# Optimization experiments

Measured on AMD Instinct MI355X. Metric: run time of the kernel, lower is better.

Reference implementation:

```python
import jax, jax.numpy as jnp
import numpy as np

N = 100000   # nodes
E = 1600000  # edges
F = 256      # feature_dim
H = 64       # hidden_dim == out_channels
HEADS = 1


def setup_inputs() -> dict:
    key = jax.random.key(0)
    ks = jax.random.split(key, 12)
    x = jax.random.normal(ks[0], (N, F), dtype=jnp.float32)
    edge_index = jax.random.randint(ks[1], (2, E), 0, N, dtype=jnp.int32)
    s = 0.05
    params = {
        'W_proj': jax.random.normal(ks[2], (F, H), dtype=jnp.float32) * s,
        'b_proj': jnp.zeros((H,), dtype=jnp.float32),
        'Wq1': jax.random.normal(ks[3], (H, HEADS * H), dtype=jnp.float32) * s,
        'Wk1': jax.random.normal(ks[4], (H, HEADS * H), dtype=jnp.float32) * s,
        'Wv1': jax.random.normal(ks[5], (H, HEADS * H), dtype=jnp.float32) * s,
        'Wq2': jax.random.normal(ks[6], (H, HEADS * H), dtype=jnp.float32) * s,
        'Wk2': jax.random.normal(ks[7], (H, HEADS * H), dtype=jnp.float32) * s,
        'Wv2': jax.random.normal(ks[8], (H, HEADS * H), dtype=jnp.float32) * s,
        'W_sig': jax.random.normal(ks[9], (H, 1), dtype=jnp.float32) * s,
        'b_sig': jnp.zeros((1,), dtype=jnp.float32),
    }
    return {'x': x, 'edge_index': edge_index, **params}


def _gat_layer(x, src, dst, Wq, Wk, Wv):
    # x: [N, H]; src/dst: [E] (edge_index[0]=source j, edge_index[1]=dest i)
    n = x.shape[0]
    q = (x @ Wq).reshape(n, HEADS, H)
    k = (x @ Wk).reshape(n, HEADS, H)
    v = (x @ Wv).reshape(n, HEADS, H)
    # edge-wise scores: (q_i * k_j).sum(-1) / sqrt(out_channels)
    scores = jnp.einsum('ehc,ehc->eh', q[dst], k[src]) / np.float32(np.sqrt(H))
    alpha = jax.nn.relu(scores)                                  # [E, HEADS]
    # segment softmax over destination neighborhoods (numerically stable)
    m = jax.ops.segment_max(alpha, dst, num_segments=n)          # [N, HEADS]
    m = jnp.where(jnp.isfinite(m), m, jnp.float32(0.0))
    e = jnp.exp(alpha - m[dst])
    denom = jax.ops.segment_sum(e, dst, num_segments=n)
    a = e / (denom[dst] + jnp.float32(1e-16))                    # [E, HEADS]
    # scatter-weighted sum of values to destinations
    out = jax.ops.segment_sum(v[src] * a[:, :, None], dst, num_segments=n)
    return out.mean(axis=1), a                                   # [N, H], [E, HEADS]


def reference(x, edge_index, W_proj, b_proj, Wq1, Wk1, Wv1, Wq2, Wk2, Wv2, W_sig, b_sig):
    src, dst = edge_index[0], edge_index[1]
    h = jax.nn.gelu(x @ W_proj + b_proj, approximate=False)
    h, attn1 = _gat_layer(h, src, dst, Wq1, Wk1, Wv1)
    h = jax.nn.gelu(h, approximate=False)
    h, attn2 = _gat_layer(h, src, dst, Wq2, Wk2, Wv2)
    signals = h @ W_sig + b_sig                                  # [N, 1]
    return signals, attn1, attn2
```

## Files before the change

kernel.cpp:

```cpp
#include <hip/hip_runtime.h>
#include <math.h>

#define FF 256
#define HH 64

typedef __attribute__((ext_vector_type(8))) short short8;
typedef __attribute__((ext_vector_type(8))) unsigned short ushort8;
typedef __attribute__((ext_vector_type(4))) float f32x4;

__device__ __forceinline__ float gelu_f(float x) {
    return 0.5f * x * (1.0f + erff(x * 0.70710678118654752f));
}

__device__ __forceinline__ unsigned short bf16rne(float f) {
    unsigned u = __float_as_uint(f);
    unsigned r = u + 0x7FFFu + ((u >> 16) & 1u);
    return (unsigned short)(r >> 16);
}
__device__ __forceinline__ float bf16tof(unsigned short s) {
    return __uint_as_float(((unsigned)s) << 16);
}

__device__ __forceinline__ void bf16split(float f, short& hi, short& lo) {
    unsigned u = __float_as_uint(f);
    unsigned r = u + 0x7FFFu + ((u >> 16) & 1u);
    hi = (short)(r >> 16);
    float fh = __uint_as_float(r & 0xFFFF0000u);
    float fl = f - fh;
    unsigned u2 = __float_as_uint(fl);
    unsigned r2 = u2 + 0x7FFFu + ((u2 >> 16) & 1u);
    lo = (short)(r2 >> 16);
}

__global__ __launch_bounds__(256) void k_wprep(
        const float* __restrict__ Wp,
        const float* __restrict__ Wq1, const float* __restrict__ Wk1, const float* __restrict__ Wv1,
        const float* __restrict__ Wq2, const float* __restrict__ Wk2, const float* __restrict__ Wv2,
        short* __restrict__ wf) {
    int total = 16384 + 6 * 4096;
    for (int gid = blockIdx.x * 256 + threadIdx.x; gid < total; gid += gridDim.x * 256) {
        const float* W;
        int fid, hibase, lobase;
        if (gid < 16384) {
            W = Wp; fid = gid; hibase = 0; lobase = 16384;
        } else {
            int t = gid - 16384;
            int m = t >> 12;
            fid = t & 4095;
            switch (m) {
                case 0: W = Wq1; break;
                case 1: W = Wk1; break;
                case 2: W = Wv1; break;
                case 3: W = Wq2; break;
                case 4: W = Wk2; break;
                default: W = Wv2; break;
            }
            hibase = 32768 + m * 8192;
            lobase = hibase + 4096;
        }
        int j    = fid & 7;
        int lane = (fid >> 3) & 63;
        int ct   = (fid >> 9) & 3;
        int s    = fid >> 11;
        int k    = s * 32 + (lane >> 4) * 8 + j;
        int col  = ct * 16 + (lane & 15);
        short hi, lo;
        bf16split(W[k * HH + col], hi, lo);
        wf[hibase + fid] = hi;
        wf[lobase + fid] = lo;
    }
}

__global__ __launch_bounds__(256) void k_degree(const int* __restrict__ dst,
        int* __restrict__ deg, int* __restrict__ rank, int E) {
    int e0 = (blockIdx.x * 256 + threadIdx.x) * 4;
    if (e0 + 3 < E) {
        int4 d4 = *reinterpret_cast<const int4*>(dst + e0);
        int4 r4;
        r4.x = atomicAdd(&deg[d4.x], 1);
        r4.y = atomicAdd(&deg[d4.y], 1);
        r4.z = atomicAdd(&deg[d4.z], 1);
        r4.w = atomicAdd(&deg[d4.w], 1);
        *reinterpret_cast<int4*>(rank + e0) = r4;
    } else {
        for (int e = e0; e < E; ++e) rank[e] = atomicAdd(&deg[dst[e]], 1);
    }
}

__global__ __launch_bounds__(256) void k_scan1(const int* __restrict__ deg,
        int* __restrict__ out, int* __restrict__ bsums, int n) {
    __shared__ int lds[256];
    int t = threadIdx.x;
    int base = blockIdx.x * 1024 + t * 4;
    int v0 = (base     < n) ? deg[base]     : 0;
    int v1 = (base + 1 < n) ? deg[base + 1] : 0;
    int v2 = (base + 2 < n) ? deg[base + 2] : 0;
    int v3 = (base + 3 < n) ? deg[base + 3] : 0;
    int s = v0 + v1 + v2 + v3;
    int val = s;
    lds[t] = val;
    __syncthreads();
    #pragma unroll
    for (int off = 1; off < 256; off <<= 1) {
        int tmp = (t >= off) ? lds[t - off] : 0;
        __syncthreads();
        val += tmp;
        lds[t] = val;
        __syncthreads();
    }
    if (t == 255) bsums[blockIdx.x] = val;
    int excl = val - s;
    if (base     < n) out[base]     = excl;
    if (base + 1 < n) out[base + 1] = excl + v0;
    if (base + 2 < n) out[base + 2] = excl + v0 + v1;
    if (base + 3 < n) out[base + 3] = excl + v0 + v1 + v2;
}

__global__ __launch_bounds__(256) void k_scan2(const int* __restrict__ bsums,
        int* __restrict__ boffs, int nb) {
    __shared__ int lds[256];
    int t = threadIdx.x;
    int s = (t < nb) ? bsums[t] : 0;
    int val = s;
    lds[t] = val;
    __syncthreads();
    #pragma unroll
    for (int off = 1; off < 256; off <<= 1) {
        int tmp = (t >= off) ? lds[t - off] : 0;
        __syncthreads();
        val += tmp;
        lds[t] = val;
        __syncthreads();
    }
    if (t < nb) boffs[t] = val - s;
}

__global__ __launch_bounds__(256) void k_scan3(int* __restrict__ rowptr,
        const int* __restrict__ boffs, int n, int E) {
    int i = blockIdx.x * 256 + threadIdx.x;
    if (i < n) rowptr[i] += boffs[i >> 10];
    if (i == n) rowptr[n] = E;
}

__global__ __launch_bounds__(256) void k_fill(const int* __restrict__ src,
        const int* __restrict__ dst, const int* __restrict__ rowptr,
        const int* __restrict__ rank,
        int* __restrict__ esrc, int* __restrict__ inv, int E) {
    int e0 = (blockIdx.x * 256 + threadIdx.x) * 4;
    if (e0 + 3 < E) {
        int4 d4 = *reinterpret_cast<const int4*>(dst + e0);
        int4 s4 = *reinterpret_cast<const int4*>(src + e0);
        int4 r4 = *reinterpret_cast<const int4*>(rank + e0);
        int p0 = rowptr[d4.x] + r4.x;
        int p1 = rowptr[d4.y] + r4.y;
        int p2 = rowptr[d4.z] + r4.z;
        int p3 = rowptr[d4.w] + r4.w;
        esrc[p0] = s4.x;
        esrc[p1] = s4.y;
        esrc[p2] = s4.z;
        esrc[p3] = s4.w;
        *reinterpret_cast<int4*>(inv + e0) = (int4){p0, p1, p2, p3};
    } else {
        for (int e = e0; e < E; ++e) {
            int pos = rowptr[dst[e]] + rank[e];
            esrc[pos] = src[e];
            inv[e] = pos;
        }
    }
}

__global__ __launch_bounds__(256) void k_attn(const float* __restrict__ ecsr,
        const int* __restrict__ inv, float* __restrict__ attn, int E) {
    int e0 = (blockIdx.x * 256 + threadIdx.x) * 4;
    if (e0 + 3 < E) {
        int4 i4 = *reinterpret_cast<const int4*>(inv + e0);
        float4 a;
        a.x = ecsr[i4.x]; a.y = ecsr[i4.y]; a.z = ecsr[i4.z]; a.w = ecsr[i4.w];
        *reinterpret_cast<float4*>(attn + e0) = a;
    } else {
        for (int e = e0; e < E; ++e) attn[e] = ecsr[inv[e]];
    }
}

__global__ __launch_bounds__(256) void k_proj(const float* __restrict__ x,
        const short* __restrict__ wf, const float* __restrict__ b,
        float* __restrict__ h, int n) {
    int lane = threadIdx.x & 63;
    int w    = threadIdx.x >> 6;
    int m    = lane & 15, g = lane >> 4;
    int rowc = min(blockIdx.x * 64 + w * 16 + m, n - 1);
    const float* xrow = x + (size_t)rowc * FF + g * 8;
    const short* wlo = wf + 16384;
    f32x4 acc[4];
    #pragma unroll
    for (int ct = 0; ct < 4; ++ct) acc[ct] = (f32x4){0.f, 0.f, 0.f, 0.f};
    #pragma unroll
    for (int s = 0; s < 8; ++s) {
        float4 a0 = *reinterpret_cast<const float4*>(xrow + s * 32);
        float4 a1 = *reinterpret_cast<const float4*>(xrow + s * 32 + 4);
        float av[8] = {a0.x, a0.y, a0.z, a0.w, a1.x, a1.y, a1.z, a1.w};
        short8 ah, al;
        #pragma unroll
        for (int j = 0; j < 8; ++j) { short hi, lo; bf16split(av[j], hi, lo); ah[j] = hi; al[j] = lo; }
        #pragma unroll
        for (int ct = 0; ct < 4; ++ct) {
            int fo = ((s * 4 + ct) * 64 + lane) * 8;
            short8 bh = *reinterpret_cast<const short8*>(wf + fo);
            short8 bl = *reinterpret_cast<const short8*>(wlo + fo);
            acc[ct] = __builtin_amdgcn_mfma_f32_16x16x32_bf16(ah, bh, acc[ct], 0, 0, 0);
            acc[ct] = __builtin_amdgcn_mfma_f32_16x16x32_bf16(al, bh, acc[ct], 0, 0, 0);
            acc[ct] = __builtin_amdgcn_mfma_f32_16x16x32_bf16(ah, bl, acc[ct], 0, 0, 0);
        }
    }
    int orow0 = blockIdx.x * 64 + w * 16 + g * 4;
    #pragma unroll
    for (int ct = 0; ct < 4; ++ct) {
        int col = ct * 16 + m;
        float bias = b[col];
        #pragma unroll
        for (int r = 0; r < 4; ++r) {
            int row = orow0 + r;
            if (row < n) h[(size_t)row * HH + col] = gelu_f(acc[ct][r] + bias);
        }
    }
}

__global__ __launch_bounds__(256) void k_qkv(const float* __restrict__ hsrc,
        const short* __restrict__ wfq, const short* __restrict__ wfk, const short* __restrict__ wfv,
        float* __restrict__ q, unsigned short* __restrict__ kv, int n) {
    int lane = threadIdx.x & 63;
    int w    = threadIdx.x >> 6;
    int m    = lane & 15, g = lane >> 4;
    int rowc = min(blockIdx.x * 64 + w * 16 + m, n - 1);
    const float* hrow = hsrc + (size_t)rowc * HH + g * 8;
    f32x4 aq[4], ak[4], av_[4];
    #pragma unroll
    for (int ct = 0; ct < 4; ++ct) {
        aq[ct] = (f32x4){0.f, 0.f, 0.f, 0.f};
        ak[ct] = (f32x4){0.f, 0.f, 0.f, 0.f};
        av_[ct] = (f32x4){0.f, 0.f, 0.f, 0.f};
    }
    #pragma unroll
    for (int s = 0; s < 2; ++s) {
        float4 a0 = *reinterpret_cast<const float4*>(hrow + s * 32);
        float4 a1 = *reinterpret_cast<const float4*>(hrow + s * 32 + 4);
        float avv[8] = {a0.x, a0.y, a0.z, a0.w, a1.x, a1.y, a1.z, a1.w};
        short8 ah, al;
        #pragma unroll
        for (int j = 0; j < 8; ++j) { short hi, lo; bf16split(avv[j], hi, lo); ah[j] = hi; al[j] = lo; }
        #pragma unroll
        for (int ct = 0; ct < 4; ++ct) {
            int fo = ((s * 4 + ct) * 64 + lane) * 8;
            short8 qh = *reinterpret_cast<const short8*>(wfq + fo);
            short8 ql = *reinterpret_cast<const short8*>(wfq + 4096 + fo);
            short8 kh = *reinterpret_cast<const short8*>(wfk + fo);
            short8 kl = *reinterpret_cast<const short8*>(wfk + 4096 + fo);
            short8 vh = *reinterpret_cast<const short8*>(wfv + fo);
            short8 vl = *reinterpret_cast<const short8*>(wfv + 4096 + fo);
            aq[ct] = __builtin_amdgcn_mfma_f32_16x16x32_bf16(ah, qh, aq[ct], 0, 0, 0);
            aq[ct] = __builtin_amdgcn_mfma_f32_16x16x32_bf16(al, qh, aq[ct], 0, 0, 0);
            aq[ct] = __builtin_amdgcn_mfma_f32_16x16x32_bf16(ah, ql, aq[ct], 0, 0, 0);
            ak[ct] = __builtin_amdgcn_mfma_f32_16x16x32_bf16(ah, kh, ak[ct], 0, 0, 0);
            ak[ct] = __builtin_amdgcn_mfma_f32_16x16x32_bf16(al, kh, ak[ct], 0, 0, 0);
            ak[ct] = __builtin_amdgcn_mfma_f32_16x16x32_bf16(ah, kl, ak[ct], 0, 0, 0);
            av_[ct] = __builtin_amdgcn_mfma_f32_16x16x32_bf16(ah, vh, av_[ct], 0, 0, 0);
            av_[ct] = __builtin_amdgcn_mfma_f32_16x16x32_bf16(al, vh, av_[ct], 0, 0, 0);
            av_[ct] = __builtin_amdgcn_mfma_f32_16x16x32_bf16(ah, vl, av_[ct], 0, 0, 0);
        }
    }
    int orow0 = blockIdx.x * 64 + w * 16 + g * 4;
    #pragma unroll
    for (int ct = 0; ct < 4; ++ct) {
        int col = ct * 16 + m;
        int cb  = (col >> 3) * 16 + (col & 7);
        #pragma unroll
        for (int r = 0; r < 4; ++r) {
            int row = orow0 + r;
            if (row < n) {
                q[(size_t)row * HH + col]       = aq[ct][r];
                kv[(size_t)row * 128 + cb]      = bf16rne(ak[ct][r]);
                kv[(size_t)row * 128 + cb + 8]  = bf16rne(av_[ct][r]);
            }
        }
    }
}

template<bool LAST>
__global__ __launch_bounds__(256) void k_edge(
        const float* __restrict__ q, const unsigned short* __restrict__ kv,
        const int* __restrict__ rowptr,
        const int* __restrict__ esrc,
        float* __restrict__ ecsr,
        float* __restrict__ hout,
        float* __restrict__ signals,
        const float* __restrict__ Wsig, const float* __restrict__ bsig,
        int n) {
    int node = blockIdx.x * 4 + (threadIdx.x >> 6);
    if (node >= n) return;
    int lane = threadIdx.x & 63;
    int li = lane & 7, g = lane >> 3;
    int start = rowptr[node], end = rowptr[node + 1];
    int deg = end - start;
    float qf[8];
    {
        float4 q0 = *reinterpret_cast<const float4*>(q + (size_t)node * HH + li * 8);
        float4 q1 = *reinterpret_cast<const float4*>(q + (size_t)node * HH + li * 8 + 4);
        qf[0] = q0.x; qf[1] = q0.y; qf[2] = q0.z; qf[3] = q0.w;
        qf[4] = q1.x; qf[5] = q1.y; qf[6] = q1.z; qf[7] = q1.w;
    }
    int p0 = start + lane;
    int el = (p0 < end) ? esrc[p0] : 0;

    float acc[8] = {0.f, 0.f, 0.f, 0.f, 0.f, 0.f, 0.f, 0.f};
    float s = 0.f;
    for (int c = 0; c < deg; c += 16) {
        int idx0 = c + g, idx1 = c + 8 + g;
        bool v0 = idx0 < deg, v1 = idx1 < deg;
        int sv0, sv1;
        if (c + 16 <= 64) {
            sv0 = __shfl(el, idx0);
            sv1 = __shfl(el, idx1);
        } else {
            sv0 = v0 ? esrc[start + idx0] : 0;
            sv1 = v1 ? esrc[start + idx1] : 0;
        }
        const unsigned short* b0 = kv + (size_t)sv0 * 128 + li * 16;
        const unsigned short* b1 = kv + (size_t)sv1 * 128 + li * 16;
        ushort8 k0 = *reinterpret_cast<const ushort8*>(b0);
        ushort8 w0 = *reinterpret_cast<const ushort8*>(b0 + 8);
        ushort8 k1 = *reinterpret_cast<const ushort8*>(b1);
        ushort8 w1 = *reinterpret_cast<const ushort8*>(b1 + 8);
        float d0 = 0.f, d1 = 0.f;
        #pragma unroll
        for (int j = 0; j < 8; ++j) {
            d0 = fmaf(qf[j], bf16tof(k0[j]), d0);
            d1 = fmaf(qf[j], bf16tof(k1[j]), d1);
        }
        d0 += __shfl_xor(d0, 1); d1 += __shfl_xor(d1, 1);
        d0 += __shfl_xor(d0, 2); d1 += __shfl_xor(d1, 2);
        d0 += __shfl_xor(d0, 4); d1 += __shfl_xor(d1, 4);
        float e0 = v0 ? __expf(fmaxf(d0 * 0.125f, 0.f)) : 0.f;
        float e1 = v1 ? __expf(fmaxf(d1 * 0.125f, 0.f)) : 0.f;
        s += e0 + e1;
        if (v0 && li == 0) ecsr[start + idx0] = e0;
        if (v1 && li == 0) ecsr[start + idx1] = e1;
        #pragma unroll
        for (int j = 0; j < 8; ++j) {
            acc[j] = fmaf(e0, bf16tof(w0[j]), acc[j]);
            acc[j] = fmaf(e1, bf16tof(w1[j]), acc[j]);
        }
    }
    #pragma unroll
    for (int off = 8; off < 64; off <<= 1) {
        s += __shfl_xor(s, off);
        #pragma unroll
        for (int j = 0; j < 8; ++j) acc[j] += __shfl_xor(acc[j], off);
    }
    float inv = 1.0f / (s + 1e-16f);

    if (!LAST) {
        if (g == 0) {
            float4 o0, o1;
            o0.x = gelu_f(acc[0] * inv); o0.y = gelu_f(acc[1] * inv);
            o0.z = gelu_f(acc[2] * inv); o0.w = gelu_f(acc[3] * inv);
            o1.x = gelu_f(acc[4] * inv); o1.y = gelu_f(acc[5] * inv);
            o1.z = gelu_f(acc[6] * inv); o1.w = gelu_f(acc[7] * inv);
            *reinterpret_cast<float4*>(hout + (size_t)node * HH + li * 8)     = o0;
            *reinterpret_cast<float4*>(hout + (size_t)node * HH + li * 8 + 4) = o1;
        }
    } else {
        float4 w0 = *reinterpret_cast<const float4*>(Wsig + li * 8);
        float4 w1 = *reinterpret_cast<const float4*>(Wsig + li * 8 + 4);
        float t = acc[0] * w0.x + acc[1] * w0.y + acc[2] * w0.z + acc[3] * w0.w
                + acc[4] * w1.x + acc[5] * w1.y + acc[6] * w1.z + acc[7] * w1.w;
        t *= inv;
        t += __shfl_xor(t, 1);
        t += __shfl_xor(t, 2);
        t += __shfl_xor(t, 4);
        if (lane == 0) signals[node] = t + bsig[0];
    }
    for (int p = p0; p < end; p += 64)
        ecsr[p] *= inv;
}

extern "C" void kernel_launch(void* const* d_in, const int* in_sizes, int n_in,
                              void* d_out, int out_size, void* d_ws, size_t ws_size,
                              hipStream_t stream) {
    const float* x   = (const float*)d_in[0];
    const int*   ei  = (const int*)  d_in[1];
    const float* Wp  = (const float*)d_in[2];
    const float* bp  = (const float*)d_in[3];
    const float* Wq1 = (const float*)d_in[4];
    const float* Wk1 = (const float*)d_in[5];
    const float* Wv1 = (const float*)d_in[6];
    const float* Wq2 = (const float*)d_in[7];
    const float* Wk2 = (const float*)d_in[8];
    const float* Wv2 = (const float*)d_in[9];
    const float* Wsg = (const float*)d_in[10];
    const float* bsg = (const float*)d_in[11];

    const int N = in_sizes[0] / FF;
    const int E = in_sizes[1] / 2;
    const int* src = ei;
    const int* dst = ei + E;

    char* ws = (char*)d_ws;
    size_t off = 0;
    auto alloc = [&](size_t bytes) -> void* {
        void* p = ws + off;
        off += (bytes + 255) & ~(size_t)255;
        return p;
    };
    float* q           = (float*)alloc((size_t)N * HH * 4);
    unsigned short* kv = (unsigned short*)alloc((size_t)N * 128 * 2);
    float* h           = (float*)alloc((size_t)N * HH * 4);
    float* ecsr        = (float*)alloc((size_t)E * 4);
    int* inv           = (int*)alloc((size_t)E * 4);
    int* esrc          = (int*)alloc((size_t)E * 4);
    int* rank          = (int*)alloc((size_t)E * 4);
    int* deg           = (int*)alloc((size_t)N * 4);
    int* rowptr        = (int*)alloc((size_t)(N + 1) * 4);
    int* bsums         = (int*)alloc(256 * 4);
    int* boffs         = (int*)alloc(256 * 4);
    short* wf          = (short*)alloc((size_t)81920 * 2);

    float* out     = (float*)d_out;
    float* signals = out;
    float* attn1   = out + N;
    float* attn2   = out + N + E;

    k_wprep<<<64, 256, 0, stream>>>(Wp, Wq1, Wk1, Wv1, Wq2, Wk2, Wv2, wf);

    hipMemsetAsync(deg, 0, (size_t)N * 4, stream);
    int e4Blocks = ((E + 3) / 4 + 255) / 256;
    k_degree<<<e4Blocks, 256, 0, stream>>>(dst, deg, rank, E);
    int nb = (N + 1023) / 1024;
    k_scan1<<<nb, 256, 0, stream>>>(deg, rowptr, bsums, N);
    k_scan2<<<1, 256, 0, stream>>>(bsums, boffs, nb);
    k_scan3<<<(N + 1 + 255) / 256, 256, 0, stream>>>(rowptr, boffs, N, E);
    k_fill<<<e4Blocks, 256, 0, stream>>>(src, dst, rowptr, rank, esrc, inv, E);

    int gemmBlocks = (N + 63) / 64;

    k_proj<<<gemmBlocks, 256, 0, stream>>>(x, wf, bp, h, N);

    const short* wfbase = wf + 32768;
    k_qkv<<<gemmBlocks, 256, 0, stream>>>(h, wfbase, wfbase + 8192, wfbase + 16384,
            q, kv, N);
    k_edge<false><<<(N + 3) / 4, 256, 0, stream>>>(q, kv, rowptr, esrc,
            ecsr, h, nullptr, nullptr, nullptr, N);
    k_attn<<<e4Blocks, 256, 0, stream>>>(ecsr, inv, attn1, E);

    k_qkv<<<gemmBlocks, 256, 0, stream>>>(h, wfbase + 24576, wfbase + 32768, wfbase + 40960,
            q, kv, N);
    k_edge<true><<<(N + 3) / 4, 256, 0, stream>>>(q, kv, rowptr, esrc,
            ecsr, nullptr, signals, Wsg, bsg, N);
    k_attn<<<e4Blocks, 256, 0, stream>>>(ecsr, inv, attn2, E);
}
```

Measured before the change: 359.7 us.

## Use fp16 packed math for edge attention, drop split-bf16 activations, move gelu into qkv

Stores q, k and v as fp16 and computes the edge dot products and value accumulation with packed half2 FMAs. This halves the q traffic and doubles the arithmetic per instruction in the gather-bound edge kernel. The qkv GEMM now rounds its activations to a single bf16 instead of a hi/lo split, cutting MFMAs from nine to six per tile. GELU moves from the producers into the qkv input path and uses a polynomial erf approximation. The costs are reduced accuracy from fp16 accumulation of attention-weighted values (overflow or precision risk for large degree sums) and from the approximate erf.

```diff
diff --git a/kernel.cpp b/kernel.cpp
--- a/kernel.cpp
+++ b/kernel.cpp
@@ -1,24 +1,27 @@
 #include <hip/hip_runtime.h>
+#include <hip/hip_fp16.h>
 #include <math.h>
 
 #define FF 256
 #define HH 64
 
 typedef __attribute__((ext_vector_type(8))) short short8;
-typedef __attribute__((ext_vector_type(8))) unsigned short ushort8;
 typedef __attribute__((ext_vector_type(4))) float f32x4;
 
 __device__ __forceinline__ float gelu_f(float x) {
-    return 0.5f * x * (1.0f + erff(x * 0.70710678118654752f));
+    float ax = fabsf(x) * 0.70710678118654752f;
+    float t = __builtin_amdgcn_rcpf(fmaf(0.3275911f, ax, 1.0f));
+    float poly = t * fmaf(t, fmaf(t, fmaf(t, fmaf(t, 1.061405429f, -1.453152027f),
+                  1.421413741f), -0.284496736f), 0.254829592f);
+    float er = 1.0f - poly * __expf(-ax * ax);
+    er = (x < 0.f) ? -er : er;
+    return 0.5f * x * (1.0f + er);
 }
 
 __device__ __forceinline__ unsigned short bf16rne(float f) {
     unsigned u = __float_as_uint(f);
     unsigned r = u + 0x7FFFu + ((u >> 16) & 1u);
     return (unsigned short)(r >> 16);
-}
-__device__ __forceinline__ float bf16tof(unsigned short s) {
-    return __uint_as_float(((unsigned)s) << 16);
 }
 
 __device__ __forceinline__ void bf16split(float f, short& hi, short& lo) {
@@ -30,6 +33,13 @@
     unsigned u2 = __float_as_uint(fl);
     unsigned r2 = u2 + 0x7FFFu + ((u2 >> 16) & 1u);
     lo = (short)(r2 >> 16);
+}
+
+__device__ __forceinline__ __half2 shfl_xor_h2(__half2 v, int off) {
+    union { __half2 h; int i; } u;
+    u.h = v;
+    u.i = __shfl_xor(u.i, off, 64);
+    return u.h;
 }
 
 __global__ __launch_bounds__(256) void k_wprep(
@@ -220,14 +230,14 @@
         #pragma unroll
         for (int r = 0; r < 4; ++r) {
             int row = orow0 + r;
-            if (row < n) h[(size_t)row * HH + col] = gelu_f(acc[ct][r] + bias);
+            if (row < n) h[(size_t)row * HH + col] = acc[ct][r] + bias;
         }
     }
 }
 
 __global__ __launch_bounds__(256) void k_qkv(const float* __restrict__ hsrc,
         const short* __restrict__ wfq, const short* __restrict__ wfk, const short* __restrict__ wfv,
-        float* __restrict__ q, unsigned short* __restrict__ kv, int n) {
+        __half* __restrict__ qh, __half* __restrict__ kv, int n) {
     int lane = threadIdx.x & 63;
     int w    = threadIdx.x >> 6;
     int m    = lane & 15, g = lane >> 4;
@@ -245,27 +255,24 @@
         float4 a0 = *reinterpret_cast<const float4*>(hrow + s * 32);
         float4 a1 = *reinterpret_cast<const float4*>(hrow + s * 32 + 4);
         float avv[8] = {a0.x, a0.y, a0.z, a0.w, a1.x, a1.y, a1.z, a1.w};
-        short8 ah, al;
-        #pragma unroll
-        for (int j = 0; j < 8; ++j) { short hi, lo; bf16split(avv[j], hi, lo); ah[j] = hi; al[j] = lo; }
+        short8 ah;
+        #pragma unroll
+        for (int j = 0; j < 8; ++j) ah[j] = (short)bf16rne(gelu_f(avv[j]));
         #pragma unroll
         for (int ct = 0; ct < 4; ++ct) {
             int fo = ((s * 4 + ct) * 64 + lane) * 8;
-            short8 qh = *reinterpret_cast<const short8*>(wfq + fo);
-            short8 ql = *reinterpret_cast<const short8*>(wfq + 4096 + fo);
-            short8 kh = *reinterpret_cast<const short8*>(wfk + fo);
-            short8 kl = *reinterpret_cast<const short8*>(wfk + 4096 + fo);
-            short8 vh = *reinterpret_cast<const short8*>(wfv + fo);
-            short8 vl = *reinterpret_cast<const short8*>(wfv + 4096 + fo);
-            aq[ct] = __builtin_amdgcn_mfma_f32_16x16x32_bf16(ah, qh, aq[ct], 0, 0, 0);
-            aq[ct] = __builtin_amdgcn_mfma_f32_16x16x32_bf16(al, qh, aq[ct], 0, 0, 0);
-            aq[ct] = __builtin_amdgcn_mfma_f32_16x16x32_bf16(ah, ql, aq[ct], 0, 0, 0);
-            ak[ct] = __builtin_amdgcn_mfma_f32_16x16x32_bf16(ah, kh, ak[ct], 0, 0, 0);
-            ak[ct] = __builtin_amdgcn_mfma_f32_16x16x32_bf16(al, kh, ak[ct], 0, 0, 0);
-            ak[ct] = __builtin_amdgcn_mfma_f32_16x16x32_bf16(ah, kl, ak[ct], 0, 0, 0);
-            av_[ct] = __builtin_amdgcn_mfma_f32_16x16x32_bf16(ah, vh, av_[ct], 0, 0, 0);
-            av_[ct] = __builtin_amdgcn_mfma_f32_16x16x32_bf16(al, vh, av_[ct], 0, 0, 0);
-            av_[ct] = __builtin_amdgcn_mfma_f32_16x16x32_bf16(ah, vl, av_[ct], 0, 0, 0);
+            short8 qh8 = *reinterpret_cast<const short8*>(wfq + fo);
+            short8 ql8 = *reinterpret_cast<const short8*>(wfq + 4096 + fo);
+            short8 kh8 = *reinterpret_cast<const short8*>(wfk + fo);
+            short8 kl8 = *reinterpret_cast<const short8*>(wfk + 4096 + fo);
+            short8 vh8 = *reinterpret_cast<const short8*>(wfv + fo);
+            short8 vl8 = *reinterpret_cast<const short8*>(wfv + 4096 + fo);
+            aq[ct] = __builtin_amdgcn_mfma_f32_16x16x32_bf16(ah, qh8, aq[ct], 0, 0, 0);
+            aq[ct] = __builtin_amdgcn_mfma_f32_16x16x32_bf16(ah, ql8, aq[ct], 0, 0, 0);
+            ak[ct] = __builtin_amdgcn_mfma_f32_16x16x32_bf16(ah, kh8, ak[ct], 0, 0, 0);
+            ak[ct] = __builtin_amdgcn_mfma_f32_16x16x32_bf16(ah, kl8, ak[ct], 0, 0, 0);
+            av_[ct] = __builtin_amdgcn_mfma_f32_16x16x32_bf16(ah, vh8, av_[ct], 0, 0, 0);
+            av_[ct] = __builtin_amdgcn_mfma_f32_16x16x32_bf16(ah, vl8, av_[ct], 0, 0, 0);
         }
     }
     int orow0 = blockIdx.x * 64 + w * 16 + g * 4;
@@ -277,9 +284,9 @@
         for (int r = 0; r < 4; ++r) {
             int row = orow0 + r;
             if (row < n) {
-                q[(size_t)row * HH + col]       = aq[ct][r];
-                kv[(size_t)row * 128 + cb]      = bf16rne(ak[ct][r]);
-                kv[(size_t)row * 128 + cb + 8]  = bf16rne(av_[ct][r]);
+                qh[(size_t)row * HH + col]     = __float2half(aq[ct][r]);
+                kv[(size_t)row * 128 + cb]     = __float2half(ak[ct][r]);
+                kv[(size_t)row * 128 + cb + 8] = __float2half(av_[ct][r]);
             }
         }
     }
@@ -287,7 +294,7 @@
 
 template<bool LAST>
 __global__ __launch_bounds__(256) void k_edge(
-        const float* __restrict__ q, const unsigned short* __restrict__ kv,
+        const __half* __restrict__ qarr, const __half* __restrict__ kv,
         const int* __restrict__ rowptr,
         const int* __restrict__ esrc,
         float* __restrict__ ecsr,
@@ -301,17 +308,19 @@
     int li = lane & 7, g = lane >> 3;
     int start = rowptr[node], end = rowptr[node + 1];
     int deg = end - start;
-    float qf[8];
+    __half2 q2[4];
     {
-        float4 q0 = *reinterpret_cast<const float4*>(q + (size_t)node * HH + li * 8);
-        float4 q1 = *reinterpret_cast<const float4*>(q + (size_t)node * HH + li * 8 + 4);
-        qf[0] = q0.x; qf[1] = q0.y; qf[2] = q0.z; qf[3] = q0.w;
-        qf[4] = q1.x; qf[5] = q1.y; qf[6] = q1.z; qf[7] = q1.w;
+        union { uint4 u; __half2 h[4]; } Q;
+        Q.u = *reinterpret_cast<const uint4*>(qarr + (size_t)node * HH + li * 8);
+        #pragma unroll
+        for (int j = 0; j < 4; ++j) q2[j] = Q.h[j];
     }
     int p0 = start + lane;
     int el = (p0 < end) ? esrc[p0] : 0;
 
-    float acc[8] = {0.f, 0.f, 0.f, 0.f, 0.f, 0.f, 0.f, 0.f};
+    __half2 acc2[4];
+    #pragma unroll
+    for (int j = 0; j < 4; ++j) acc2[j] = __float2half2_rn(0.f);
     float s = 0.f;
     for (int c = 0; c < deg; c += 16) {
         int idx0 = c + g, idx1 = c + 8 + g;
@@ -324,18 +333,22 @@
             sv0 = v0 ? esrc[start + idx0] : 0;
             sv1 = v1 ? esrc[start + idx1] : 0;
         }
-        const unsigned short* b0 = kv + (size_t)sv0 * 128 + li * 16;
-        const unsigned short* b1 = kv + (size_t)sv1 * 128 + li * 16;
-        ushort8 k0 = *reinterpret_cast<const ushort8*>(b0);
-        ushort8 w0 = *reinterpret_cast<const ushort8*>(b0 + 8);
-        ushort8 k1 = *reinterpret_cast<const ushort8*>(b1);
-        ushort8 w1 = *reinterpret_cast<const ushort8*>(b1 + 8);
-        float d0 = 0.f, d1 = 0.f;
-        #pragma unroll
-        for (int j = 0; j < 8; ++j) {
-            d0 = fmaf(qf[j], bf16tof(k0[j]), d0);
-            d1 = fmaf(qf[j], bf16tof(k1[j]), d1);
-        }
+        const __half* b0 = kv + (size_t)sv0 * 128 + li * 16;
+        const __half* b1 = kv + (size_t)sv1 * 128 + li * 16;
+        union { uint4 u; __half2 h[4]; } K0, V0, K1, V1;
+        K0.u = *reinterpret_cast<const uint4*>(b0);
+        V0.u = *reinterpret_cast<const uint4*>(b0 + 8);
+        K1.u = *reinterpret_cast<const uint4*>(b1);
+        V1.u = *reinterpret_cast<const uint4*>(b1 + 8);
+        __half2 d20 = __float2half2_rn(0.f);
+        __half2 d21 = __float2half2_rn(0.f);
+        #pragma unroll
+        for (int j = 0; j < 4; ++j) {
+            d20 = __hfma2(q2[j], K0.h[j], d20);
+            d21 = __hfma2(q2[j], K1.h[j], d21);
+        }
+        float d0 = __low2float(d20) + __high2float(d20);
+        float d1 = __low2float(d21) + __high2float(d21);
         d0 += __shfl_xor(d0, 1); d1 += __shfl_xor(d1, 1);
         d0 += __shfl_xor(d0, 2); d1 += __shfl_xor(d1, 2);
         d0 += __shfl_xor(d0, 4); d1 += __shfl_xor(d1, 4);
@@ -344,35 +357,42 @@
         s += e0 + e1;
         if (v0 && li == 0) ecsr[start + idx0] = e0;
         if (v1 && li == 0) ecsr[start + idx1] = e1;
-        #pragma unroll
-        for (int j = 0; j < 8; ++j) {
-            acc[j] = fmaf(e0, bf16tof(w0[j]), acc[j]);
-            acc[j] = fmaf(e1, bf16tof(w1[j]), acc[j]);
+        __half2 e20 = __float2half2_rn(e0);
+        __half2 e21 = __float2half2_rn(e1);
+        #pragma unroll
+        for (int j = 0; j < 4; ++j) {
+            acc2[j] = __hfma2(e20, V0.h[j], acc2[j]);
+            acc2[j] = __hfma2(e21, V1.h[j], acc2[j]);
         }
     }
     #pragma unroll
     for (int off = 8; off < 64; off <<= 1) {
         s += __shfl_xor(s, off);
         #pragma unroll
-        for (int j = 0; j < 8; ++j) acc[j] += __shfl_xor(acc[j], off);
+        for (int j = 0; j < 4; ++j)
+            acc2[j] = __hadd2(acc2[j], shfl_xor_h2(acc2[j], off));
     }
     float inv = 1.0f / (s + 1e-16f);
+    float af[8];
+    #pragma unroll
+    for (int j = 0; j < 4; ++j) {
+        af[2 * j]     = __low2float(acc2[j]);
+        af[2 * j + 1] = __high2float(acc2[j]);
+    }
 
     if (!LAST) {
         if (g == 0) {
             float4 o0, o1;
-            o0.x = gelu_f(acc[0] * inv); o0.y = gelu_f(acc[1] * inv);
-            o0.z = gelu_f(acc[2] * inv); o0.w = gelu_f(acc[3] * inv);
-            o1.x = gelu_f(acc[4] * inv); o1.y = gelu_f(acc[5] * inv);
-            o1.z = gelu_f(acc[6] * inv); o1.w = gelu_f(acc[7] * inv);
+            o0.x = af[0] * inv; o0.y = af[1] * inv; o0.z = af[2] * inv; o0.w = af[3] * inv;
+            o1.x = af[4] * inv; o1.y = af[5] * inv; o1.z = af[6] * inv; o1.w = af[7] * inv;
             *reinterpret_cast<float4*>(hout + (size_t)node * HH + li * 8)     = o0;
             *reinterpret_cast<float4*>(hout + (size_t)node * HH + li * 8 + 4) = o1;
         }
     } else {
         float4 w0 = *reinterpret_cast<const float4*>(Wsig + li * 8);
         float4 w1 = *reinterpret_cast<const float4*>(Wsig + li * 8 + 4);
-        float t = acc[0] * w0.x + acc[1] * w0.y + acc[2] * w0.z + acc[3] * w0.w
-                + acc[4] * w1.x + acc[5] * w1.y + acc[6] * w1.z + acc[7] * w1.w;
+        float t = af[0] * w0.x + af[1] * w0.y + af[2] * w0.z + af[3] * w0.w
+                + af[4] * w1.x + af[5] * w1.y + af[6] * w1.z + af[7] * w1.w;
         t *= inv;
         t += __shfl_xor(t, 1);
         t += __shfl_xor(t, 2);
@@ -411,18 +431,18 @@
         off += (bytes + 255) & ~(size_t)255;
         return p;
     };
-    float* q           = (float*)alloc((size_t)N * HH * 4);
-    unsigned short* kv = (unsigned short*)alloc((size_t)N * 128 * 2);
-    float* h           = (float*)alloc((size_t)N * HH * 4);
-    float* ecsr        = (float*)alloc((size_t)E * 4);
-    int* inv           = (int*)alloc((size_t)E * 4);
-    int* esrc          = (int*)alloc((size_t)E * 4);
-    int* rank          = (int*)alloc((size_t)E * 4);
-    int* deg           = (int*)alloc((size_t)N * 4);
-    int* rowptr        = (int*)alloc((size_t)(N + 1) * 4);
-    int* bsums         = (int*)alloc(256 * 4);
-    int* boffs         = (int*)alloc(256 * 4);
-    short* wf          = (short*)alloc((size_t)81920 * 2);
+    __half* qh   = (__half*)alloc((size_t)N * HH * 2);
+    __half* kv   = (__half*)alloc((size_t)N * 128 * 2);
+    float* h     = (float*)alloc((size_t)N * HH * 4);
+    float* ecsr  = (float*)alloc((size_t)E * 4);
+    int* inv     = (int*)alloc((size_t)E * 4);
+    int* esrc    = (int*)alloc((size_t)E * 4);
+    int* rank    = (int*)alloc((size_t)E * 4);
+    int* deg     = (int*)alloc((size_t)N * 4);
+    int* rowptr  = (int*)alloc((size_t)(N + 1) * 4);
+    int* bsums   = (int*)alloc(256 * 4);
+    int* boffs   = (int*)alloc(256 * 4);
+    short* wf    = (short*)alloc((size_t)81920 * 2);
 
     float* out     = (float*)d_out;
     float* signals = out;
@@ -446,14 +466,14 @@
 
     const short* wfbase = wf + 32768;
     k_qkv<<<gemmBlocks, 256, 0, stream>>>(h, wfbase, wfbase + 8192, wfbase + 16384,
-            q, kv, N);
-    k_edge<false><<<(N + 3) / 4, 256, 0, stream>>>(q, kv, rowptr, esrc,
+            qh, kv, N);
+    k_edge<false><<<(N + 3) / 4, 256, 0, stream>>>(qh, kv, rowptr, esrc,
             ecsr, h, nullptr, nullptr, nullptr, N);
     k_attn<<<e4Blocks, 256, 0, stream>>>(ecsr, inv, attn1, E);
 
     k_qkv<<<gemmBlocks, 256, 0, stream>>>(h, wfbase + 24576, wfbase + 32768, wfbase + 40960,
-            q, kv, N);
-    k_edge<true><<<(N + 3) / 4, 256, 0, stream>>>(q, kv, rowptr, esrc,
+            qh, kv, N);
+    k_edge<true><<<(N + 3) / 4, 256, 0, stream>>>(qh, kv, rowptr, esrc,
             ecsr, nullptr, signals, Wsg, bsg, N);
     k_attn<<<e4Blocks, 256, 0, stream>>>(ecsr, inv, attn2, E);
 }
```

Result: faster. 341.5 us (-5.1%).
